# Performance work log

Hardware: AMD Instinct MI355X
Metric: run time of the kernel (lower is better)

## Reference

```python
import jax, jax.numpy as jnp
import numpy as np

N = 4096
IN_CH = 256
OUT_CH = 256
NUM_REL = 8


def setup_inputs() -> dict:
    key = jax.random.key(0)
    k_x, k_a, k_e, k_w = jax.random.split(key, 4)
    x = jax.random.normal(k_x, (N, IN_CH), dtype=jnp.float32)
    A = jax.random.uniform(k_a, (N, N), dtype=jnp.float32)
    edge_type = jax.random.randint(k_e, (N, N), 0, NUM_REL, dtype=jnp.int32)
    # xavier_uniform per-relation weight [R, in, out]
    limit = np.sqrt(6.0 / (IN_CH + OUT_CH))
    weight = jax.random.uniform(k_w, (NUM_REL, IN_CH, OUT_CH), dtype=jnp.float32,
                                minval=-limit, maxval=limit)
    bias = jnp.zeros((OUT_CH,), dtype=jnp.float32)
    return {"x": x, "A": A, "edge_type": edge_type, "weight": weight, "bias": bias}


def reference(x, A, edge_type, weight, bias):
    # out = sum_r ((A * [edge_type == r]) @ x) @ W_r + bias
    num_rel = weight.shape[0]
    out = jnp.zeros((x.shape[0], weight.shape[2]), dtype=x.dtype)
    for rel in range(num_rel):  # small fixed relation count
        rel_adj = A * (edge_type == rel).astype(x.dtype)   # [N, N]
        h = rel_adj @ x                                     # [N, in]
        out = out + h @ weight[rel]                         # [N, out]
    out = out + bias
    return out
```

## Files before the change

### kernel.cpp

```cpp
#include <hip/hip_runtime.h>
#include <stdint.h>


#define NN 4096

typedef __attribute__((ext_vector_type(8)))  short s16x8;
typedef __attribute__((ext_vector_type(16))) float f32x16;
typedef __attribute__((ext_vector_type(4)))  float fx4;
typedef __attribute__((ext_vector_type(4)))  int   ix4;
typedef __attribute__((ext_vector_type(4)))  unsigned int ux4;
typedef __attribute__((ext_vector_type(4)))  _Float16 h4;

union uq { ux4 u; s16x8 s; };

__device__ __forceinline__ unsigned short f2bf(float f) {
  union { float f; unsigned int u; } v; v.f = f;
  unsigned int r = v.u + 0x7fffu + ((v.u >> 16) & 1u);
  return (unsigned short)(r >> 16);
}

__device__ __forceinline__ void gld16(const void* g, void* l) {
  __builtin_amdgcn_global_load_lds(
      (const __attribute__((address_space(1))) unsigned int*)(uintptr_t)g,
      (__attribute__((address_space(3))) unsigned int*)(uintptr_t)l, 16, 0, 0);
}

__device__ __forceinline__ unsigned packAE(float a, int e) {
  unsigned ab = __float_as_uint(a) + 0x2000u;
  unsigned ex = ab >> 23;
  int el = (int)ex - 112;
  unsigned m9 = (ab >> 14) & 0x1FFu;
  unsigned v = ((unsigned)el << 9) | m9;
  if (el <= 0) v = 0;
  return (unsigned short)(((unsigned)e << 13) | (v & 0x1FFFu));
}

__global__ void k_init(const float* __restrict__ bias, float* __restrict__ out) {
  int idx = blockIdx.x * 256 + threadIdx.x;
  out[idx] = bias[idx & 255];
}

__global__ __launch_bounds__(256, 4) void k_t(const float* __restrict__ A,
                                              const int*   __restrict__ et,
                                              unsigned short* __restrict__ Apk) {
  __shared__ unsigned int lds[64 * 129];
  const int t = threadIdx.x;
  const int bt = blockIdx.x;
  const int ib = (bt & 127) * 32;
  const int byy = bt >> 7;
  const int jb = byy * 512;
  const int jgb = byy * 64;

  const int jl = (t & 127) * 4;
  const int r0 = t >> 7;
  const int jg = jl >> 3;
  const int dd = (jl & 7) >> 1;
  const float* baseA = A  + (size_t)(ib + r0) * NN + jb + jl;
  const int*   baseE = et + (size_t)(ib + r0) * NN + jb + jl;

#define LOADB(g, AA, EE) do {                                             \
    _Pragma("unroll")                                                     \
    for (int k = 0; k < 4; ++k) {                                         \
      AA[k] = *(const fx4*)(baseA + (size_t)((g) * 8 + k * 2) * NN);      \
      EE[k] = *(const ix4*)(baseE + (size_t)((g) * 8 + k * 2) * NN);      \
    }                                                                     \
  } while (0)

#define PROCB(g, AA, EE) do {                                             \
    _Pragma("unroll")                                                     \
    for (int k = 0; k < 4; ++k) {                                         \
      const int row = ((g) * 4 + k) * 2 + r0;                             \
      unsigned d0 = (unsigned)packAE(AA[k].x, EE[k].x)                    \
                  | ((unsigned)packAE(AA[k].y, EE[k].y) << 16);           \
      unsigned d1 = (unsigned)packAE(AA[k].z, EE[k].z)                    \
                  | ((unsigned)packAE(AA[k].w, EE[k].w) << 16);           \
      lds[jg * 129 + row * 4 + dd]     = d0;                              \
      lds[jg * 129 + row * 4 + dd + 1] = d1;                              \
    }                                                                     \
  } while (0)

  fx4 aP[4], aQ[4]; ix4 eP[4], eQ[4];
  LOADB(0, aP, eP);
  LOADB(1, aQ, eQ);
  PROCB(0, aP, eP);
  LOADB(2, aP, eP);
  PROCB(1, aQ, eQ);
  LOADB(3, aQ, eQ);
  PROCB(2, aP, eP);
  PROCB(3, aQ, eQ);
#undef LOADB
#undef PROCB
  __syncthreads();

  const int lh1 = (t >> 5) & 1, l31 = t & 31;
  const int wv = t >> 6;
#pragma unroll
  for (int v = 0; v < 8; ++v) {
    const int jgw = (wv * 8 + v) * 2 + lh1;
    const int base = jgw * 129 + l31 * 4;
    ux4 q;
    q.x = lds[base]; q.y = lds[base + 1]; q.z = lds[base + 2]; q.w = lds[base + 3];
    ((ux4*)Apk)[(size_t)(jgb + jgw) * NN + ib + l31] = q;
  }
}

__global__ __launch_bounds__(256, 2) void k_y(const float* __restrict__ x,
                                              const float* __restrict__ W,
                                              unsigned short* __restrict__ yt) {
  __shared__ unsigned short Wl[128 * 256];
  const int t  = threadIdx.x;
  const int j0 = blockIdx.x * 128;
  const int o0 = blockIdx.y * 16;

  {
    const int r = t >> 5, kc = t & 31;
#pragma unroll
    for (int u = 0; u < 8; ++u) {
      const int k = kc * 8 + u;
      const fx4* wp = (const fx4*)(W + ((size_t)r * 256 + k) * 256 + o0);
      fx4 w[4] = { wp[0], wp[1], wp[2], wp[3] };
#pragma unroll
      for (int i = 0; i < 16; ++i) {
        const int row = i * 8 + r;
        const int gs  = (k >> 3) ^ (row & 7);
        Wl[row * 256 + gs * 8 + (k & 7)] = f2bf(w[i >> 2][i & 3]);
      }
    }
  }
  __syncthreads();

  const int lane = t & 63, wid = t >> 6;
  const int l15 = lane & 15, lh = lane >> 4;
  const int npb = wid * 32;

  fx4 acc[8][2];
#pragma unroll
  for (int m = 0; m < 8; ++m)
#pragma unroll
    for (int n = 0; n < 2; ++n) acc[m][n] = 0.f;

  unsigned int qb[2];
#pragma unroll
  for (int n = 0; n < 2; ++n) {
    int row = npb + n * 16 + l15;
    qb[n] = (unsigned)(row * 512 + 16 * (lh ^ (row & 3))) ^ (64u * ((row >> 2) & 1));
  }
  const char* WlB = (const char*)Wl;
  const float* xb = x + (size_t)(j0 + l15) * 256 + lh * 8;

#pragma unroll
  for (int ks = 0; ks < 8; ++ks) {
    s16x8 a[8];
#pragma unroll
    for (int m = 0; m < 8; ++m) {
      const fx4* xp = (const fx4*)(xb + (size_t)m * 16 * 256 + ks * 32);
      fx4 x0 = xp[0], x1 = xp[1];
      s16x8 av;
#pragma unroll
      for (int i = 0; i < 4; ++i) av[i] = (short)f2bf(x0[i]);
#pragma unroll
      for (int i = 0; i < 4; ++i) av[4 + i] = (short)f2bf(x1[i]);
      a[m] = av;
    }
#pragma unroll
    for (int n = 0; n < 2; ++n) {
      s16x8 bb = *(const s16x8*)(WlB + (qb[n] ^ (unsigned)(ks * 64)));
#pragma unroll
      for (int m = 0; m < 8; ++m)
        acc[m][n] = __builtin_amdgcn_mfma_f32_16x16x32_bf16(a[m], bb, acc[m][n], 0, 0, 0);
    }
  }

#pragma unroll
  for (int m = 0; m < 8; ++m)
#pragma unroll
    for (int n = 0; n < 2; ++n)
#pragma unroll
      for (int q = 0; q < 4; ++q) {
        int jl = m * 16 + lh * 4 + q;
        int np = npb + n * 16 + l15;
        int o  = o0 + (np >> 3);
        yt[((size_t)(j0 + jl) * 256 + o) * 8 + (np & 7)] = f2bf(acc[m][n][q]);
      }
}

__global__ __launch_bounds__(256, 3) void k_main(const unsigned short* __restrict__ Apk,
                                                 const unsigned short* __restrict__ yt,
                                                 float* __restrict__ dstF,
                                                 _Float16* __restrict__ dstH,
                                                 int usePart) {
  __shared__ ux4 Bl[3 * 1024];
  char* Bc = (char*)Bl;
  const int t = threadIdx.x, lane = t & 63, w = t >> 6;
  const int l31 = lane & 31, lh1 = lane >> 5;
  const int wm = w >> 1, wn = w & 1;
  const int b = blockIdx.x;
  const int kz = b & 15;
  const int io = b >> 4;
  const int i0 = (io >> 1) * 128;
  const int o0 = (io & 1) * 128;
  const int jb = kz * 256;
  const int jg0 = kz * 32;

  const ux4* pA[2];
#pragma unroll
  for (int m = 0; m < 2; ++m)
    pA[m] = (const ux4*)Apk + (size_t)jg0 * NN + i0 + wm * 64 + m * 32 + l31;

  const ux4* ytg = (const ux4*)yt;
  const ux4* pB[4];
  unsigned dOff[4];
#pragma unroll
  for (int u = 0; u < 4; ++u) {
    int slot = u * 256 + t;
    pB[u] = ytg + (size_t)(jb + (slot >> 7)) * 256 + o0 + (slot & 127);
    dOff[u] = (unsigned)(slot * 16);
  }

#define ISSUE(sq, bb, ASET) do {                                          \
    _Pragma("unroll")                                                     \
    for (int u = 0; u < 4; ++u)                                           \
      gld16(pB[u] + (size_t)(sq) * 2048, Bc + (bb) * 16384 + dOff[u]);    \
    ASET[0] = pA[0][(size_t)(sq) * NN];                                   \
    ASET[1] = pA[1][(size_t)(sq) * NN];                                   \
  } while (0)

  const unsigned shA = (unsigned)(lh1 * 16);
#define BUILD(ASET, FR) do {                                              \
    _Pragma("unroll")                                                     \
    for (int m = 0; m < 2; ++m)                                           \
      _Pragma("unroll")                                                   \
      for (int ks = 0; ks < 4; ++ks) {                                    \
        unsigned u16 = (ASET[m][ks] >> shA) & 0xFFFFu;                    \
        unsigned a16 = 0x3800u | ((u16 >> 2) & 0x7FFu);                   \
        unsigned e   = u16 >> 13;                                         \
        unsigned long long sh = (unsigned long long)a16 << ((e & 3u) << 4); \
        unsigned lo = (unsigned)sh, hi = (unsigned)(sh >> 32);            \
        bool c = e < 4;                                                   \
        ux4 q; q.x = c ? lo : 0u; q.y = c ? hi : 0u;                      \
        q.z = c ? 0u : lo; q.w = c ? 0u : hi;                             \
        FR[m][ks].u = q;                                                  \
      }                                                                   \
  } while (0)

  unsigned rB[2];
#pragma unroll
  for (int n = 0; n < 2; ++n)
    rB[n] = (unsigned)((wn * 64 + n * 32 + l31) * 16);

#define COMPUTE(bb, FR) do {                                              \
    const unsigned base = (unsigned)((bb) * 16384) + (unsigned)(lh1 * 2048); \
    _Pragma("unroll")                                                     \
    for (int ks = 0; ks < 4; ++ks) {                                      \
      uq b0, b1;                                                          \
      b0.u = *(const ux4*)(Bc + base + (unsigned)(ks * 4096) + rB[0]);    \
      b1.u = *(const ux4*)(Bc + base + (unsigned)(ks * 4096) + rB[1]);    \
      _Pragma("unroll")                                                   \
      for (int m = 0; m < 2; ++m) {                                       \
        acc[m][0] = __builtin_amdgcn_mfma_f32_32x32x16_bf16(FR[m][ks].s, b0.s, acc[m][0], 0, 0, 0); \
        acc[m][1] = __builtin_amdgcn_mfma_f32_32x32x16_bf16(FR[m][ks].s, b1.s, acc[m][1], 0, 0, 0); \
      }                                                                   \
    }                                                                     \
  } while (0)

  f32x16 acc[2][2];
#pragma unroll
  for (int m = 0; m < 2; ++m)
#pragma unroll
    for (int n = 0; n < 2; ++n) acc[m][n] = 0.f;

  ux4 aE[2], aO[2];
  uq frE[2][4], frO[2][4];

  ISSUE(0, 0, aE);
  ISSUE(1, 1, aO);

  for (int s = 0; s < 32; s += 2) {
    const int sq2 = (s + 2 < 32) ? s + 2 : 31;
    const int sq3 = (s + 3 < 32) ? s + 3 : 31;
    const int b0 = s % 3, b1 = (s + 1) % 3, b2 = (s + 2) % 3;
    asm volatile("s_waitcnt vmcnt(6)" ::: "memory");
    __builtin_amdgcn_s_barrier();
    BUILD(aE, frE);
    ISSUE(sq2, b2, aE);
    __builtin_amdgcn_s_setprio(1);
    COMPUTE(b0, frE);
    __builtin_amdgcn_s_setprio(0);
    asm volatile("s_waitcnt vmcnt(6)" ::: "memory");
    __builtin_amdgcn_s_barrier();
    BUILD(aO, frO);
    ISSUE(sq3, b0, aO);
    __builtin_amdgcn_s_setprio(1);
    COMPUTE(b1, frO);
    __builtin_amdgcn_s_setprio(0);
  }
  asm volatile("s_waitcnt vmcnt(0)" ::: "memory");

  if (usePart) {
    _Float16* pp = dstH + ((size_t)kz << 20);
#pragma unroll
    for (int m = 0; m < 2; ++m)
#pragma unroll
      for (int n = 0; n < 2; ++n)
#pragma unroll
        for (int q = 0; q < 16; ++q) {
          int gi = i0 + wm * 64 + m * 32 + (q & 3) + 8 * (q >> 2) + 4 * lh1;
          int go = o0 + wn * 64 + n * 32 + l31;
          pp[(size_t)gi * 256 + go] = (_Float16)acc[m][n][q];
        }
  } else {
#pragma unroll
    for (int m = 0; m < 2; ++m)
#pragma unroll
      for (int n = 0; n < 2; ++n)
#pragma unroll
        for (int q = 0; q < 16; ++q) {
          int gi = i0 + wm * 64 + m * 32 + (q & 3) + 8 * (q >> 2) + 4 * lh1;
          int go = o0 + wn * 64 + n * 32 + l31;
          atomicAdd(dstF + (size_t)gi * 256 + go, acc[m][n][q]);
        }
  }
#undef ISSUE
#undef BUILD
#undef COMPUTE
}

__global__ __launch_bounds__(256) void k_red(const _Float16* __restrict__ part,
                                             const float* __restrict__ bias,
                                             float* __restrict__ out) {
  int idx = blockIdx.x * 256 + threadIdx.x;
  fx4 s = *(const fx4*)(bias + ((idx << 2) & 255));
#pragma unroll
  for (int k = 0; k < 16; ++k) {
    h4 h = *(const h4*)(part + ((size_t)k << 20) + (size_t)idx * 4);
    s.x += (float)h.x; s.y += (float)h.y; s.z += (float)h.z; s.w += (float)h.w;
  }
  ((fx4*)out)[idx] = s;
}

extern "C" void kernel_launch(void* const* d_in, const int* in_sizes, int n_in,
                              void* d_out, int out_size, void* d_ws, size_t ws_size,
                              hipStream_t stream) {
  const float* x    = (const float*)d_in[0];
  const float* A    = (const float*)d_in[1];
  const int*   et   = (const int*)d_in[2];
  const float* W    = (const float*)d_in[3];
  const float* bias = (const float*)d_in[4];
  float* out = (float*)d_out;

  unsigned short* yt  = (unsigned short*)d_ws;
  unsigned short* Apk = (unsigned short*)((char*)d_ws + ((size_t)16 << 20));
  _Float16*       pp  = (_Float16*)((char*)d_ws + ((size_t)48 << 20));

  const bool usePart = ws_size >= ((size_t)80 << 20);

  k_t<<<dim3(1024), dim3(256), 0, stream>>>(A, et, Apk);
  k_y<<<dim3(32, 16), dim3(256), 0, stream>>>(x, W, yt);
  if (usePart) {
    k_main<<<dim3(1024), dim3(256), 0, stream>>>(Apk, yt, out, pp, 1);
    k_red<<<dim3(1024), dim3(256), 0, stream>>>(pp, bias, out);
  } else {
    k_init<<<dim3(4096), dim3(256), 0, stream>>>(bias, out);
    k_main<<<dim3(1024), dim3(256), 0, stream>>>(Apk, yt, out, pp, 0);
  }
}
```

Before: 152.0 us.

## Give each wave private LDS B buffers and remove block barriers

Restructures the B-tile staging so that each wave loads its own 64-column slice into a private, double-buffered LDS region, which removes the workgroup barriers in the main loop. The triple-buffered shared layout is replaced, and the refill is issued after compute on the same buffer. B data is now loaded redundantly by waves sharing columns, and LDS use grows to 64KB, so occupancy drops from 3 to 2 blocks per CU.

```diff
diff --git a/kernel.cpp b/kernel.cpp
--- a/kernel.cpp
+++ b/kernel.cpp
@@ -184,12 +184,12 @@
       }
 }
 
-__global__ __launch_bounds__(256, 3) void k_main(const unsigned short* __restrict__ Apk,
+__global__ __launch_bounds__(256, 2) void k_main(const unsigned short* __restrict__ Apk,
                                                  const unsigned short* __restrict__ yt,
                                                  float* __restrict__ dstF,
                                                  _Float16* __restrict__ dstH,
                                                  int usePart) {
-  __shared__ ux4 Bl[3 * 1024];
+  __shared__ ux4 Bl[4096];
   char* Bc = (char*)Bl;
   const int t = threadIdx.x, lane = t & 63, w = t >> 6;
   const int l31 = lane & 31, lh1 = lane >> 5;
@@ -202,25 +202,21 @@
   const int jb = kz * 256;
   const int jg0 = kz * 32;
 
+  const unsigned wbase = (unsigned)(w * 16384);
+
   const ux4* pA[2];
 #pragma unroll
   for (int m = 0; m < 2; ++m)
     pA[m] = (const ux4*)Apk + (size_t)jg0 * NN + i0 + wm * 64 + m * 32 + l31;
 
   const ux4* ytg = (const ux4*)yt;
-  const ux4* pB[4];
-  unsigned dOff[4];
-#pragma unroll
-  for (int u = 0; u < 4; ++u) {
-    int slot = u * 256 + t;
-    pB[u] = ytg + (size_t)(jb + (slot >> 7)) * 256 + o0 + (slot & 127);
-    dOff[u] = (unsigned)(slot * 16);
-  }
-
-#define ISSUE(sq, bb, ASET) do {                                          \
-    _Pragma("unroll")                                                     \
-    for (int u = 0; u < 4; ++u)                                           \
-      gld16(pB[u] + (size_t)(sq) * 2048, Bc + (bb) * 16384 + dOff[u]);    \
+  const ux4* pBbase = ytg + (size_t)jb * 256 + o0 + wn * 64 + lane;
+
+#define ISSUE(sq, bf, ASET) do {                                          \
+    _Pragma("unroll")                                                     \
+    for (int u = 0; u < 8; ++u)                                           \
+      gld16(pBbase + (size_t)(sq) * 2048 + u * 256,                       \
+            Bc + wbase + (unsigned)((bf) * 8192 + u * 1024));             \
     ASET[0] = pA[0][(size_t)(sq) * NN];                                   \
     ASET[1] = pA[1][(size_t)(sq) * NN];                                   \
   } while (0)
@@ -243,18 +239,14 @@
       }                                                                   \
   } while (0)
 
-  unsigned rB[2];
-#pragma unroll
-  for (int n = 0; n < 2; ++n)
-    rB[n] = (unsigned)((wn * 64 + n * 32 + l31) * 16);
-
-#define COMPUTE(bb, FR) do {                                              \
-    const unsigned base = (unsigned)((bb) * 16384) + (unsigned)(lh1 * 2048); \
+#define COMPUTE(bf, FR) do {                                              \
+    const unsigned base = wbase + (unsigned)((bf) * 8192)                 \
+                        + (unsigned)(lh1 * 1024) + (unsigned)(l31 * 16);  \
     _Pragma("unroll")                                                     \
     for (int ks = 0; ks < 4; ++ks) {                                      \
       uq b0, b1;                                                          \
-      b0.u = *(const ux4*)(Bc + base + (unsigned)(ks * 4096) + rB[0]);    \
-      b1.u = *(const ux4*)(Bc + base + (unsigned)(ks * 4096) + rB[1]);    \
+      b0.u = *(const ux4*)(Bc + base + (unsigned)(ks * 2048));            \
+      b1.u = *(const ux4*)(Bc + base + (unsigned)(ks * 2048 + 512));      \
       _Pragma("unroll")                                                   \
       for (int m = 0; m < 2; ++m) {                                       \
         acc[m][0] = __builtin_amdgcn_mfma_f32_32x32x16_bf16(FR[m][ks].s, b0.s, acc[m][0], 0, 0, 0); \
@@ -278,21 +270,14 @@
   for (int s = 0; s < 32; s += 2) {
     const int sq2 = (s + 2 < 32) ? s + 2 : 31;
     const int sq3 = (s + 3 < 32) ? s + 3 : 31;
-    const int b0 = s % 3, b1 = (s + 1) % 3, b2 = (s + 2) % 3;
-    asm volatile("s_waitcnt vmcnt(6)" ::: "memory");
-    __builtin_amdgcn_s_barrier();
+    asm volatile("s_waitcnt vmcnt(10)" ::: "memory");
     BUILD(aE, frE);
-    ISSUE(sq2, b2, aE);
-    __builtin_amdgcn_s_setprio(1);
-    COMPUTE(b0, frE);
-    __builtin_amdgcn_s_setprio(0);
-    asm volatile("s_waitcnt vmcnt(6)" ::: "memory");
-    __builtin_amdgcn_s_barrier();
+    COMPUTE(0, frE);
+    ISSUE(sq2, 0, aE);
+    asm volatile("s_waitcnt vmcnt(10)" ::: "memory");
     BUILD(aO, frO);
-    ISSUE(sq3, b0, aO);
-    __builtin_amdgcn_s_setprio(1);
-    COMPUTE(b1, frO);
-    __builtin_amdgcn_s_setprio(0);
+    COMPUTE(1, frO);
+    ISSUE(sq3, 1, aO);
   }
   asm volatile("s_waitcnt vmcnt(0)" ::: "memory");
 
```

New measurement: 152.9 us. No clear change (+0.6%).
